# Kernel tuning notes

Hardware: AMD Instinct MI355X
Metric: run time of the kernel (lower is better)

## Reference

```python
import jax, jax.numpy as jnp
import numpy as np

N_NODES = 50000
N_EDGES = 800000   # avg degree ~16
IN_CH = 128
HID = 64


def setup_inputs() -> dict:
    key = jax.random.key(0)
    k0, k1, k2, k3 = jax.random.split(key, 4)
    x = jax.random.normal(k0, (N_NODES, IN_CH), dtype=jnp.float32)
    edge_index = jax.random.randint(k1, (2, N_EDGES), 0, N_NODES, dtype=jnp.int32)
    # Glorot-ish init like torch GCNConv
    W1 = jax.random.normal(k2, (IN_CH, HID), dtype=jnp.float32) / np.sqrt(IN_CH).astype(np.float32)
    b1 = jnp.zeros((HID,), dtype=jnp.float32)
    W2 = jax.random.normal(k3, (HID, HID), dtype=jnp.float32) / np.sqrt(HID).astype(np.float32)
    b2 = jnpp = jnp.zeros((HID,), dtype=jnp.float32)
    return {"x": x, "edge_index": edge_index, "W1": W1, "b1": b1, "W2": W2, "b2": b2}


def gcn_conv(x, src, dst, W, b, n):
    """GCNConv with self-loops already appended to (src, dst).
    out = D^{-1/2} (A + I) D^{-1/2} (x @ W) + b, symmetric normalization."""
    h = x @ W                                        # [N, out]
    deg = jax.ops.segment_sum(jnp.ones(src.shape, jnp.float32), dst, num_segments=n)
    dinv = jax.lax.rsqrt(jnp.maximum(deg, 1.0))      # deg >= 1 due to self-loops
    norm = dinv[src] * dinv[dst]                     # [E+N]
    msg = h[src] * norm[:, None]                     # gather + scale
    return jax.ops.segment_sum(msg, dst, num_segments=n) + b


def reference(x, edge_index, W1, b1, W2, b2):
    n = x.shape[0]
    loop = jnp.arange(n, dtype=edge_index.dtype)
    src = jnp.concatenate([edge_index[0], loop])     # add self-loops
    dst = jnp.concatenate([edge_index[1], loop])
    # encode: GCNConv -> ReLU -> GCNConv
    z = jax.nn.relu(gcn_conv(x, src, dst, W1, b1, n))
    z = gcn_conv(z, src, dst, W2, b2, n)
    # decode: gather endpoint embeddings, elementwise product, reduce over hidden
    return (z[edge_index[0]] * z[edge_index[1]]).sum(axis=1)   # [E]
```

## Files before the change

kernel.cpp:

```cpp
#include <hip/hip_runtime.h>
#include <hip/hip_fp16.h>

#define INCH 128
#define HIDC 64
#define CAP  64

typedef int            v4i __attribute__((ext_vector_type(4)));
typedef float          v4f __attribute__((ext_vector_type(4)));
typedef float          v2f __attribute__((ext_vector_type(2)));
typedef unsigned int   v4u __attribute__((ext_vector_type(4)));

__device__ inline float2 u2f(unsigned int u) {
    return __half22float2(__builtin_bit_cast(__half2, u));
}
__device__ inline unsigned int f2u(float a, float b) {
    __half2 h = __float22half2_rn(make_float2(a, b));
    return __builtin_bit_cast(unsigned int, h);
}

__global__ __launch_bounds__(128, 2) void build_gemm1_kernel(const int* __restrict__ src,
                                                             const int* __restrict__ dst,
                                                             int* __restrict__ count,
                                                             unsigned short* __restrict__ col,
                                                             const float* __restrict__ x,
                                                             const float* __restrict__ W,
                                                             __half* __restrict__ hs,
                                                             int E, int N, int GB) {
    int b = (int)blockIdx.x;
    if (b >= GB) {
        int eb = b - GB;
        int g = eb & 7;
        int chunkBase = (eb >> 3) * 2048;
        int t = (int)threadIdx.x;
        if (chunkBase + 2048 <= E) {
            v4i s4[4], d4[4];
            #pragma unroll
            for (int i = 0; i < 4; ++i) {
                int e0 = chunkBase + (i * 128 + t) * 4;
                d4[i] = *(const v4i*)(dst + e0);
                s4[i] = *(const v4i*)(src + e0);
            }
            #pragma unroll
            for (int i = 0; i < 4; ++i) {
                #pragma unroll
                for (int k = 0; k < 4; ++k) {
                    int d = d4[i][k];
                    if ((d & 7) == g) {
                        int r = atomicAdd(&count[d], 1);
                        if (r < CAP) col[(size_t)d * CAP + r] = (unsigned short)s4[i][k];
                    }
                }
            }
        } else {
            #pragma unroll
            for (int i = 0; i < 4; ++i) {
                int e0 = chunkBase + (i * 128 + t) * 4;
                for (int e = e0; e < e0 + 4 && e < E; ++e) {
                    int d = dst[e];
                    if ((d & 7) == g) {
                        int r = atomicAdd(&count[d], 1);
                        if (r < CAP) col[(size_t)d * CAP + r] = (unsigned short)src[e];
                    }
                }
            }
        }
    } else {
        int node = (b >> 1) * 128 + (int)threadIdx.x;
        int ch0 = (b & 1) * 32;
        if (node >= N) return;
        const float4* xr = (const float4*)(x + (size_t)node * INCH);
        float acc[32];
        #pragma unroll
        for (int c = 0; c < 32; ++c) acc[c] = 0.f;
        for (int kc = 0; kc < INCH / 4; ++kc) {
            float4 xk = xr[kc];
            const float* wr = W + (kc * 4) * HIDC + ch0;
            #pragma unroll
            for (int ch = 0; ch < 32; ++ch) acc[ch] = fmaf(xk.x, wr[ch], acc[ch]);
            #pragma unroll
            for (int ch = 0; ch < 32; ++ch) acc[ch] = fmaf(xk.y, wr[HIDC + ch], acc[ch]);
            #pragma unroll
            for (int ch = 0; ch < 32; ++ch) acc[ch] = fmaf(xk.z, wr[2 * HIDC + ch], acc[ch]);
            #pragma unroll
            for (int ch = 0; ch < 32; ++ch) acc[ch] = fmaf(xk.w, wr[3 * HIDC + ch], acc[ch]);
        }
        v4u hv[4];
        #pragma unroll
        for (int k = 0; k < 4; ++k) {
            #pragma unroll
            for (int e = 0; e < 4; ++e) {
                int c2 = k * 4 + e;
                hv[k][e] = f2u(acc[2 * c2], acc[2 * c2 + 1]);
            }
        }
        v4u* hr = (v4u*)(hs + (size_t)node * HIDC + ch0);
        #pragma unroll
        for (int k = 0; k < 4; ++k) hr[k] = hv[k];
    }
}

__global__ __launch_bounds__(256) void scale_kernel(const int* __restrict__ count,
                                                    __half* __restrict__ hs, int N) {
    int idx = (int)blockIdx.x * 256 + threadIdx.x;
    if (idx >= N * 8) return;
    int node = idx >> 3;
    float dn = rsqrtf((float)count[node] + 1.0f);
    v4u v = ((const v4u*)hs)[idx];
    v4u o;
    #pragma unroll
    for (int k = 0; k < 4; ++k) {
        float2 f = u2f(v[k]);
        o[k] = f2u(dn * f.x, dn * f.y);
    }
    ((v4u*)hs)[idx] = o;
}

__global__ __launch_bounds__(128, 2) void gemm2_kernel(const __half* __restrict__ agg1,
                                                       const float* __restrict__ W,
                                                       const int* __restrict__ count,
                                                       __half* __restrict__ hs, int N) {
    int node = (blockIdx.x >> 1) * 128 + threadIdx.x;
    int ch0 = (blockIdx.x & 1) * 32;
    if (node >= N) return;
    const v4u* ar = (const v4u*)(agg1 + (size_t)node * HIDC);
    float acc[32];
    #pragma unroll
    for (int c = 0; c < 32; ++c) acc[c] = 0.f;
    for (int kc = 0; kc < HIDC / 8; ++kc) {
        v4u av = ar[kc];
        #pragma unroll
        for (int k2 = 0; k2 < 4; ++k2) {
            float2 f = u2f(av[k2]);
            float v0 = fmaxf(f.x, 0.f);
            float v1 = fmaxf(f.y, 0.f);
            const float* wr = W + (kc * 8 + k2 * 2) * HIDC + ch0;
            #pragma unroll
            for (int ch = 0; ch < 32; ++ch) acc[ch] = fmaf(v0, wr[ch], acc[ch]);
            #pragma unroll
            for (int ch = 0; ch < 32; ++ch) acc[ch] = fmaf(v1, wr[HIDC + ch], acc[ch]);
        }
    }
    float dn = rsqrtf((float)count[node] + 1.0f);
    v4u hv[4];
    #pragma unroll
    for (int k = 0; k < 4; ++k) {
        #pragma unroll
        for (int e = 0; e < 4; ++e) {
            int c2 = k * 4 + e;
            hv[k][e] = f2u(dn * acc[2 * c2], dn * acc[2 * c2 + 1]);
        }
    }
    v4u* hr = (v4u*)(hs + (size_t)node * HIDC + ch0);
    #pragma unroll
    for (int k = 0; k < 4; ++k) hr[k] = hv[k];
}

__global__ __launch_bounds__(256) void aggregate_kernel(const int* __restrict__ count,
                                                        const unsigned short* __restrict__ col,
                                                        const __half* __restrict__ hs,
                                                        const float* __restrict__ bias,
                                                        __half* __restrict__ agg, int N) {
    int node = blockIdx.x * 8 + (threadIdx.x >> 5);
    int c2 = threadIdx.x & 31;
    if (node >= N) return;
    int cnt = count[node];
    int deg = cnt < CAP ? cnt : CAP;
    const unsigned int* h2p = (const unsigned int*)hs;
    float2 acc = u2f(h2p[(size_t)node * 32 + c2]);
    const unsigned short* row = col + (size_t)node * CAP;
    for (int jb = 0; jb < deg; jb += 16) {
        int s[16];
        unsigned int v[16];
        #pragma unroll
        for (int u = 0; u < 16; ++u) {
            int idx = jb + u;
            s[u] = row[idx < deg ? idx : jb];
        }
        #pragma unroll
        for (int u = 0; u < 16; ++u)
            v[u] = h2p[(size_t)s[u] * 32 + c2];
        #pragma unroll
        for (int u = 0; u < 16; ++u) {
            if (jb + u < deg) {
                float2 f = u2f(v[u]);
                acc.x += f.x; acc.y += f.y;
            }
        }
    }
    float dn = rsqrtf((float)cnt + 1.0f);
    float2 bb = *(const float2*)(bias + c2 * 2);
    ((unsigned int*)agg)[(size_t)node * 32 + c2] =
        f2u(fmaf(acc.x, dn, bb.x), fmaf(acc.y, dn, bb.y));
}

__global__ __launch_bounds__(256) void decode_kernel(const int* __restrict__ src,
                                                     const int* __restrict__ dst,
                                                     const __half* __restrict__ z,
                                                     float* __restrict__ out, int E) {
    long long tid = (long long)blockIdx.x * 256 + threadIdx.x;
    int g = (int)(tid >> 3);
    int q = threadIdx.x & 7;
    int e0 = g * 4;
    if (e0 >= E) return;
    const v4u* z8 = (const v4u*)z;
    bool full = (e0 + 3 < E);
    int s[4], d[4];
    if (full) {
        v4i sv = __builtin_nontemporal_load((const v4i*)(src + e0));
        v4i dv = __builtin_nontemporal_load((const v4i*)(dst + e0));
        s[0]=sv.x; s[1]=sv.y; s[2]=sv.z; s[3]=sv.w;
        d[0]=dv.x; d[1]=dv.y; d[2]=dv.z; d[3]=dv.w;
    } else {
        #pragma unroll
        for (int k = 0; k < 4; ++k) {
            int e = e0 + k < E ? e0 + k : e0;
            s[k] = src[e]; d[k] = dst[e];
        }
    }
    v4u a[4], b[4];
    #pragma unroll
    for (int k = 0; k < 4; ++k) a[k] = z8[(size_t)s[k] * 8 + q];
    #pragma unroll
    for (int k = 0; k < 4; ++k) b[k] = z8[(size_t)d[k] * 8 + q];
    float p[4];
    #pragma unroll
    for (int k = 0; k < 4; ++k) {
        float acc = 0.f;
        #pragma unroll
        for (int j = 0; j < 4; ++j) {
            float2 fa = u2f(a[k][j]);
            float2 fb = u2f(b[k][j]);
            acc = fmaf(fa.x, fb.x, acc);
            acc = fmaf(fa.y, fb.y, acc);
        }
        p[k] = acc;
    }
    #pragma unroll
    for (int m = 4; m; m >>= 1) {
        #pragma unroll
        for (int k = 0; k < 4; ++k) p[k] += __shfl_xor(p[k], m, 64);
    }
    if (q == 0) {
        if (full) {
            v4f r; r.x = p[0]; r.y = p[1]; r.z = p[2]; r.w = p[3];
            __builtin_nontemporal_store(r, (v4f*)(out + e0));
        } else {
            for (int k = 0; k < 4 && e0 + k < E; ++k) out[e0 + k] = p[k];
        }
    }
}

extern "C" void kernel_launch(void* const* d_in, const int* in_sizes, int n_in,
                              void* d_out, int out_size, void* d_ws, size_t ws_size,
                              hipStream_t stream) {
    const float* x  = (const float*)d_in[0];
    const int*   ei = (const int*)d_in[1];
    const float* W1 = (const float*)d_in[2];
    const float* b1 = (const float*)d_in[3];
    const float* W2 = (const float*)d_in[4];
    const float* b2 = (const float*)d_in[5];
    float* out = (float*)d_out;

    const int hid  = in_sizes[3];
    const int inch = in_sizes[2] / hid;
    const int N    = in_sizes[0] / inch;
    const int E    = in_sizes[1] / 2;
    const int* srcp = ei;
    const int* dstp = ei + E;

    char* p = (char*)d_ws;
    auto alloc = [&](size_t bytes) { char* r = p; p += (bytes + 255) & ~(size_t)255; return r; };
    int*            count = (int*)alloc((size_t)N * 4);
    unsigned short* col   = (unsigned short*)alloc((size_t)N * CAP * 2);
    __half*         h1s   = (__half*)alloc((size_t)N * HIDC * 2);
    __half*         h2s   = (__half*)alloc((size_t)N * HIDC * 2);
    __half*         zt    = (__half*)alloc((size_t)N * HIDC * 2);
    __half*         agg1  = (__half*)alloc((size_t)N * HIDC * 2);

    (void)hipMemsetAsync(count, 0, (size_t)N * 4, stream);

    int GB  = 2 * ((N + 127) / 128);
    int EBK = 8 * ((E + 2047) / 2048);
    build_gemm1_kernel<<<GB + EBK, 128, 0, stream>>>(srcp, dstp, count, col,
                                                     x, W1, h1s, E, N, GB);
    scale_kernel<<<(N * 8 + 255) / 256, 256, 0, stream>>>(count, h1s, N);

    aggregate_kernel<<<(N + 7) / 8, 256, 0, stream>>>(count, col, h1s, b1, agg1, N);
    gemm2_kernel<<<GB, 128, 0, stream>>>(agg1, W2, count, h2s, N);
    aggregate_kernel<<<(N + 7) / 8, 256, 0, stream>>>(count, col, h2s, b2, zt, N);

    long long groups = ((long long)E + 3) / 4;
    long long blocksD = (groups * 8 + 255) / 256;
    decode_kernel<<<(int)blocksD, 256, 0, stream>>>(srcp, dstp, zt, out, E);
}
```

Before: 204.2 us.

## Fuse layer-1 aggregation with the second GEMM via shared-memory weights

Merges the first neighbor-aggregation pass and the second dense transform into one kernel. Each block stages W2 (16KB) in LDS, aggregates eight nodes across wavefronts, and writes the post-bias ReLU rows to LDS. Each wave then computes its own node's 64-channel output from LDS and writes the normalized fp16 result. This removes one kernel launch and the fp16 agg1 intermediate round trip through global memory. In exchange every block reloads W2 into LDS, and the GEMM now uses fp32 activations instead of fp16. It relies on a per-wave lgkmcnt wait rather than a barrier, which is valid only because each wave reads back its own rows.

```diff
diff --git a/kernel.cpp b/kernel.cpp
--- a/kernel.cpp
+++ b/kernel.cpp
@@ -7,7 +7,6 @@
 
 typedef int            v4i __attribute__((ext_vector_type(4)));
 typedef float          v4f __attribute__((ext_vector_type(4)));
-typedef float          v2f __attribute__((ext_vector_type(2)));
 typedef unsigned int   v4u __attribute__((ext_vector_type(4)));
 
 __device__ inline float2 u2f(unsigned int u) {
@@ -115,44 +114,73 @@
     ((v4u*)hs)[idx] = o;
 }
 
-__global__ __launch_bounds__(128, 2) void gemm2_kernel(const __half* __restrict__ agg1,
-                                                       const float* __restrict__ W,
-                                                       const int* __restrict__ count,
-                                                       __half* __restrict__ hs, int N) {
-    int node = (blockIdx.x >> 1) * 128 + threadIdx.x;
-    int ch0 = (blockIdx.x & 1) * 32;
+__global__ __launch_bounds__(256) void agg1_gemm2_kernel(const int* __restrict__ count,
+                                                         const unsigned short* __restrict__ col,
+                                                         const __half* __restrict__ hs,
+                                                         const float* __restrict__ b1,
+                                                         const float* __restrict__ W2,
+                                                         __half* __restrict__ out, int N) {
+    __shared__ float sW2[HIDC * HIDC];
+    __shared__ float sAgg[8 * HIDC];
+    int t = (int)threadIdx.x;
+    {
+        const float4* w4 = (const float4*)W2;
+        float4* s4 = (float4*)sW2;
+        #pragma unroll
+        for (int i = 0; i < 4; ++i) s4[t + 256 * i] = w4[t + 256 * i];
+    }
+    __syncthreads();
+
+    int nl = t >> 5;
+    int node = (int)blockIdx.x * 8 + nl;
+    int c2 = t & 31;
     if (node >= N) return;
-    const v4u* ar = (const v4u*)(agg1 + (size_t)node * HIDC);
-    float acc[32];
-    #pragma unroll
-    for (int c = 0; c < 32; ++c) acc[c] = 0.f;
-    for (int kc = 0; kc < HIDC / 8; ++kc) {
-        v4u av = ar[kc];
-        #pragma unroll
-        for (int k2 = 0; k2 < 4; ++k2) {
-            float2 f = u2f(av[k2]);
-            float v0 = fmaxf(f.x, 0.f);
-            float v1 = fmaxf(f.y, 0.f);
-            const float* wr = W + (kc * 8 + k2 * 2) * HIDC + ch0;
-            #pragma unroll
-            for (int ch = 0; ch < 32; ++ch) acc[ch] = fmaf(v0, wr[ch], acc[ch]);
-            #pragma unroll
-            for (int ch = 0; ch < 32; ++ch) acc[ch] = fmaf(v1, wr[HIDC + ch], acc[ch]);
-        }
-    }
-    float dn = rsqrtf((float)count[node] + 1.0f);
-    v4u hv[4];
-    #pragma unroll
-    for (int k = 0; k < 4; ++k) {
-        #pragma unroll
-        for (int e = 0; e < 4; ++e) {
-            int c2 = k * 4 + e;
-            hv[k][e] = f2u(dn * acc[2 * c2], dn * acc[2 * c2 + 1]);
-        }
-    }
-    v4u* hr = (v4u*)(hs + (size_t)node * HIDC + ch0);
-    #pragma unroll
-    for (int k = 0; k < 4; ++k) hr[k] = hv[k];
+    int cnt = count[node];
+    int deg = cnt < CAP ? cnt : CAP;
+    const unsigned int* h2p = (const unsigned int*)hs;
+    float2 acc = u2f(h2p[(size_t)node * 32 + c2]);
+    const unsigned short* row = col + (size_t)node * CAP;
+    for (int jb = 0; jb < deg; jb += 16) {
+        int s[16];
+        unsigned int v[16];
+        #pragma unroll
+        for (int u = 0; u < 16; ++u) {
+            int idx = jb + u;
+            s[u] = row[idx < deg ? idx : jb];
+        }
+        #pragma unroll
+        for (int u = 0; u < 16; ++u)
+            v[u] = h2p[(size_t)s[u] * 32 + c2];
+        #pragma unroll
+        for (int u = 0; u < 16; ++u) {
+            if (jb + u < deg) {
+                float2 f = u2f(v[u]);
+                acc.x += f.x; acc.y += f.y;
+            }
+        }
+    }
+    float dn = rsqrtf((float)cnt + 1.0f);
+    float2 bb = *(const float2*)(b1 + c2 * 2);
+    float px = fmaxf(fmaf(acc.x, dn, bb.x), 0.f);
+    float py = fmaxf(fmaf(acc.y, dn, bb.y), 0.f);
+    ((float2*)sAgg)[nl * 32 + c2] = make_float2(px, py);
+    __asm__ volatile("s_waitcnt lgkmcnt(0)" ::: "memory");
+
+    float o0 = 0.f, o1 = 0.f;
+    const float4* aF4 = (const float4*)(sAgg + nl * HIDC);
+    #pragma unroll
+    for (int kk = 0; kk < 16; ++kk) {
+        float4 a4 = aF4[kk];
+        float2 w0 = ((const float2*)(sW2 + (kk * 4 + 0) * HIDC))[c2];
+        float2 w1 = ((const float2*)(sW2 + (kk * 4 + 1) * HIDC))[c2];
+        float2 w2 = ((const float2*)(sW2 + (kk * 4 + 2) * HIDC))[c2];
+        float2 w3 = ((const float2*)(sW2 + (kk * 4 + 3) * HIDC))[c2];
+        o0 = fmaf(a4.x, w0.x, o0); o1 = fmaf(a4.x, w0.y, o1);
+        o0 = fmaf(a4.y, w1.x, o0); o1 = fmaf(a4.y, w1.y, o1);
+        o0 = fmaf(a4.z, w2.x, o0); o1 = fmaf(a4.z, w2.y, o1);
+        o0 = fmaf(a4.w, w3.x, o0); o1 = fmaf(a4.w, w3.y, o1);
+    }
+    ((unsigned int*)out)[(size_t)node * 32 + c2] = f2u(o0 * dn, o1 * dn);
 }
 
 __global__ __launch_bounds__(256) void aggregate_kernel(const int* __restrict__ count,
@@ -275,7 +303,6 @@
     __half*         h1s   = (__half*)alloc((size_t)N * HIDC * 2);
     __half*         h2s   = (__half*)alloc((size_t)N * HIDC * 2);
     __half*         zt    = (__half*)alloc((size_t)N * HIDC * 2);
-    __half*         agg1  = (__half*)alloc((size_t)N * HIDC * 2);
 
     (void)hipMemsetAsync(count, 0, (size_t)N * 4, stream);
 
@@ -285,8 +312,8 @@
                                                      x, W1, h1s, E, N, GB);
     scale_kernel<<<(N * 8 + 255) / 256, 256, 0, stream>>>(count, h1s, N);
 
-    aggregate_kernel<<<(N + 7) / 8, 256, 0, stream>>>(count, col, h1s, b1, agg1, N);
-    gemm2_kernel<<<GB, 128, 0, stream>>>(agg1, W2, count, h2s, N);
+    agg1_gemm2_kernel<<<(N + 7) / 8, 256, 0, stream>>>(count, col, h1s, b1, W2, h2s, N);
+
     aggregate_kernel<<<(N + 7) / 8, 256, 0, stream>>>(count, col, h2s, b2, zt, N);
 
     long long groups = ((long long)E + 3) / 4;
```

Result: faster. 197.1 us (-3.5%).
